# Kernel tuning notes

Measured on AMD Instinct MI355X. Metric: run time of the kernel, lower is better.

Reference implementation:

```python
import jax, jax.numpy as jnp
import numpy as np

B, L, D, H = 2, 2048, 1024, 16
HD = D // H  # head_dim = 64


def setup_inputs() -> dict:
    key = jax.random.key(0)
    ks = jax.random.split(key, 6)
    return {
        "q": jax.random.normal(ks[0], (B, L, D), dtype=jnp.float32),
        "k": jax.random.normal(ks[1], (B, L, D), dtype=jnp.float32),
        "v": jax.random.normal(ks[2], (B, L, D), dtype=jnp.float32),
        "Wq": jax.random.normal(ks[3], (D, D), dtype=jnp.float32) * (D ** -0.5),
        "Wk": jax.random.normal(ks[4], (D, D), dtype=jnp.float32) * (D ** -0.5),
        "Wv": jax.random.normal(ks[5], (D, D), dtype=jnp.float32) * (D ** -0.5),
    }


def reference(q, k, v, Wq, Wk, Wv):
    # nn.Linear(bias=False): y = x @ W.T ; then split heads -> [B,H,L,HD]
    def proj(x, W):
        return (x @ W.T).reshape(B, L, H, HD).transpose(0, 2, 1, 3)

    Q = proj(q, Wq)
    K = proj(k, Wk)
    V = proj(v, Wv)
    scale = HD ** -0.5
    idx = jnp.arange(L)
    # flex_attention score_mod: score + (q_idx - kv_idx), applied after scaling
    bias = (idx[:, None] - idx[None, :]).astype(q.dtype)  # [L, L]
    scores = jnp.einsum('bhqd,bhkd->bhqk', Q, K) * scale + bias
    attn = jax.nn.softmax(scores, axis=-1)
    out = jnp.einsum('bhqk,bhkd->bhqd', attn, V)
    # 'b h l d -> b l (h d)'
    return out.transpose(0, 2, 1, 3).reshape(B, L, D)
```

## Files before the change

### kernel.cpp

```cpp
#include <hip/hip_runtime.h>

#define DEVFN __device__ __forceinline__

typedef __attribute__((ext_vector_type(8))) short bf16x8;
typedef __attribute__((ext_vector_type(4))) float f32x4;

constexpr int cB = 2, cL = 2048, cD = 1024, cH = 16, cHD = 64;
constexpr int ELE   = 4194304;
constexpr int WELE  = 1048576;
constexpr int KWIN  = 128;
constexpr int SLICE = 2 * KWIN * cD;

#if __has_builtin(__builtin_amdgcn_exp2f)
#define EXP2F(x) __builtin_amdgcn_exp2f(x)
#else
#define EXP2F(x) __expf(0.6931471805599453f * (x))
#endif

DEVFN unsigned short hu(float f) {
  return (unsigned short)((__float_as_uint(f) + 0x8000u) >> 16);
}
DEVFN unsigned pkhu(float a, float b) {
  unsigned ua = __float_as_uint(a) + 0x8000u;
  unsigned ub = __float_as_uint(b) + 0x8000u;
  return __builtin_amdgcn_perm(ub, ua, 0x07060302u);
}

#if __has_builtin(__builtin_amdgcn_global_load_lds)
#define HAVE_ASYNC 1
typedef const __attribute__((address_space(1))) unsigned int* gas1_t;
typedef __attribute__((address_space(3))) unsigned int* las3_t;
#define ASYNC_CP16(g, l) \
  __builtin_amdgcn_global_load_lds((gas1_t)(g), (las3_t)(l), 16, 0, 0)
#else
#define HAVE_ASYNC 0
#endif

DEVFN int swzofs(int row, int cc) { return row * 64 + (((cc) ^ (row & 7)) << 3); }

__global__ __launch_bounds__(256)
void conv_bf16(const float* __restrict__ q, const float* __restrict__ k,
               const float* __restrict__ v, const float* __restrict__ Wq,
               const float* __restrict__ Wk, const float* __restrict__ Wv,
               unsigned short* __restrict__ qb, unsigned short* __restrict__ kb,
               unsigned short* __restrict__ vb, unsigned short* __restrict__ wb) {
  const int y = blockIdx.y;
  const int i8 = (blockIdx.x * 256 + threadIdx.x) * 8;
  const float* src; unsigned short* dst; int n;
  size_t sofs = i8, dofs = i8;
  switch (y) {
    case 0:  src = q;  dst = qb;          n = ELE;  break;
    case 1:  case 2: {
      n = SLICE;
      const size_t b = (size_t)(i8 >> 17);
      sofs = b * ((size_t)cL * cD) + (i8 & (KWIN * cD - 1));
      src = (y == 1) ? k : v;  dst = (y == 1) ? kb : vb;  break;
    }
    case 3:  src = Wq; dst = wb;          n = WELE; break;
    case 4:  src = Wk; dst = wb + WELE;   n = WELE; break;
    default: src = Wv; dst = wb + 2*WELE; n = WELE; break;
  }
  if (i8 >= n) return;
  float4 a = *(const float4*)(src + sofs);
  float4 b4 = *(const float4*)(src + sofs + 4);
  uint4 o = {pkhu(a.x, a.y), pkhu(a.z, a.w), pkhu(b4.x, b4.y), pkhu(b4.z, b4.w)};
  *(uint4*)(dst + dofs) = o;
}

__global__ __launch_bounds__(256)
void proj_kv(const unsigned short* __restrict__ xk,
             const unsigned short* __restrict__ xv,
             const unsigned short* __restrict__ wAll,
             unsigned short* __restrict__ Kc,
             unsigned short* __restrict__ Vc) {
  __shared__ __align__(16) unsigned short As[128 * 64];
  __shared__ __align__(16) unsigned short Bs[64 * 64];
  const int tid = threadIdx.x;
  const int wv = tid >> 6, lane = tid & 63, id = lane & 15, quad = lane >> 4;
  const int wr = wv >> 1, wc = wv & 1;
  const int rl = lane >> 3, cc = (lane & 7) ^ rl;

  const int bx = blockIdx.x;
  int mode, M0, N0;
  const unsigned short *A, *B;
  unsigned short* outp;
  if (bx < 32) {
    mode = 1; A = xk; B = wAll + WELE; outp = Kc;
    M0 = (bx & 1) * KWIN;
    N0 = (bx >> 1) * 64;
  } else {
    const int t = bx - 32;
    mode = 2; A = wAll + 2 * WELE; B = xv; outp = Vc;
    M0 = (t & 7) * 128;
    const int y = t >> 3;
    N0 = (y >> 1) * KWIN + (y & 1) * 64;
  }

  f32x4 acc[4][2];
#pragma unroll
  for (int i = 0; i < 4; ++i)
#pragma unroll
    for (int j = 0; j < 2; ++j) acc[i][j] = (f32x4){0.f, 0.f, 0.f, 0.f};

  for (int k0 = 0; k0 < cD; k0 += 64) {
#if HAVE_ASYNC
    __syncthreads();
#pragma unroll
    for (int c = 0; c < 4; ++c)
      ASYNC_CP16(A + (size_t)(M0 + c * 32 + wv * 8 + rl) * cD + k0 + cc * 8,
                 &As[(c * 32 + wv * 8) * 64]);
#pragma unroll
    for (int c = 0; c < 2; ++c)
      ASYNC_CP16(B + (size_t)(N0 + c * 32 + wv * 8 + rl) * cD + k0 + cc * 8,
                 &Bs[(c * 32 + wv * 8) * 64]);
    __syncthreads();
#else
    uint4 ra[4], rb[2];
#pragma unroll
    for (int c = 0; c < 4; ++c)
      ra[c] = *(const uint4*)(A + (size_t)(M0 + c * 32 + wv * 8 + rl) * cD + k0 + cc * 8);
#pragma unroll
    for (int c = 0; c < 2; ++c)
      rb[c] = *(const uint4*)(B + (size_t)(N0 + c * 32 + wv * 8 + rl) * cD + k0 + cc * 8);
    __syncthreads();
#pragma unroll
    for (int c = 0; c < 4; ++c) *(uint4*)&As[(c * 32 + wv * 8) * 64 + lane * 8] = ra[c];
#pragma unroll
    for (int c = 0; c < 2; ++c) *(uint4*)&Bs[(c * 32 + wv * 8) * 64 + lane * 8] = rb[c];
    __syncthreads();
#endif

#pragma unroll
    for (int ks = 0; ks < 2; ++ks) {
      bf16x8 af[4], bfr[2];
#pragma unroll
      for (int mi = 0; mi < 4; ++mi)
        af[mi] = *(const bf16x8*)&As[swzofs(wr * 64 + mi * 16 + id, ks * 4 + quad)];
#pragma unroll
      for (int ni = 0; ni < 2; ++ni)
        bfr[ni] = *(const bf16x8*)&Bs[swzofs(wc * 32 + ni * 16 + id, ks * 4 + quad)];
#pragma unroll
      for (int mi = 0; mi < 4; ++mi)
#pragma unroll
        for (int ni = 0; ni < 2; ++ni)
          acc[mi][ni] = __builtin_amdgcn_mfma_f32_16x16x32_bf16(
              af[mi], bfr[ni], acc[mi][ni], 0, 0, 0);
    }
  }

#pragma unroll
  for (int mi = 0; mi < 4; ++mi) {
#pragma unroll
    for (int ni = 0; ni < 2; ++ni) {
#pragma unroll
      for (int rg = 0; rg < 4; ++rg) {
        const int mr = M0 + wr * 64 + mi * 16 + quad * 4 + rg;
        const int nc = N0 + wc * 32 + ni * 16 + id;
        size_t idx;
        if (mode == 1) {
          const int b = mr >> 7, l = mr & 127, h = nc >> 6, hd = nc & 63;
          idx = ((size_t)((b * cH + h) * KWIN + l)) * cHD + hd;
        } else {
          const int h = mr >> 6, hd = mr & 63, b = nc >> 7, l = nc & 127;
          idx = ((size_t)((b * cH + h) * cHD + hd)) * KWIN + l;
        }
        outp[idx] = hu(acc[mi][ni][rg]);
      }
    }
  }
}

__global__ __launch_bounds__(512)
void fused_qattn(const unsigned short* __restrict__ Xq,
                 const unsigned short* __restrict__ Wq,
                 const unsigned short* __restrict__ Kc,
                 const unsigned short* __restrict__ Vc,
                 float* __restrict__ out) {
  __shared__ __align__(16) unsigned short lds[40960];
  unsigned short* Ks = lds + 24576;
  unsigned short* Vs = lds + 32768;
  unsigned short* Ps = lds + 16384;

  const int tid = threadIdx.x;
  const int wv = tid >> 6, lane = tid & 63, id = lane & 15, quad = lane >> 4;
  const int wr = wv >> 1, wc = wv & 1;
  const int rl = lane >> 3, cc = (lane & 7) ^ rl;
  const int bh = blockIdx.y, q0 = blockIdx.x * 128;
  const int bb = bh >> 4, h = bh & 15;
  const size_t M0 = (size_t)bb * cL + q0;
  const unsigned short* Bw = Wq + (size_t)(h * cHD) * cD;
  const unsigned short* Kb = Kc + (size_t)bh * KWIN * cHD;
  const unsigned short* Vb = Vc + (size_t)bh * cHD * KWIN;

  const int rbase = wv * 8;

#if HAVE_ASYNC
#pragma unroll
  for (int c = 0; c < 2; ++c)
    ASYNC_CP16(Kb + (size_t)(c * 64 + rbase + rl) * cHD + cc * 8,
               &Ks[(c * 64 + rbase) * 64]);
#pragma unroll
  for (int it = 0; it < 2; ++it)
    ASYNC_CP16(Vb + (size_t)(rbase + rl) * KWIN + it * 64 + cc * 8,
               &Vs[it * 4096 + rbase * 64]);
#else
  {
    uint4 kv0r = *(const uint4*)(Kb + (size_t)(rbase + rl) * cHD + cc * 8);
    uint4 kv1r = *(const uint4*)(Kb + (size_t)(64 + rbase + rl) * cHD + cc * 8);
    uint4 vv0r = *(const uint4*)(Vb + (size_t)(rbase + rl) * KWIN + cc * 8);
    uint4 vv1r = *(const uint4*)(Vb + (size_t)(rbase + rl) * KWIN + 64 + cc * 8);
    *(uint4*)&Ks[rbase * 64 + lane * 8] = kv0r;
    *(uint4*)&Ks[(64 + rbase) * 64 + lane * 8] = kv1r;
    *(uint4*)&Vs[rbase * 64 + lane * 8] = vv0r;
    *(uint4*)&Vs[4096 + rbase * 64 + lane * 8] = vv1r;
  }
#endif

#if HAVE_ASYNC
#define STAGE_TILE(buf, k0)                                                    \
  {                                                                            \
    unsigned short* A_ = lds + (buf) * 8192;                                   \
    unsigned short* B_ = lds + 16384 + (buf) * 4096;                           \
    _Pragma("unroll")                                                          \
    for (int c = 0; c < 2; ++c)                                                \
      ASYNC_CP16(Xq + (M0 + c * 64 + wv * 8 + rl) * cD + (k0) + cc * 8,        \
                 &A_[(c * 64 + wv * 8) * 64]);                                 \
    ASYNC_CP16(Bw + (size_t)(wv * 8 + rl) * cD + (k0) + cc * 8,                \
               &B_[(wv * 8) * 64]);                                            \
  }
#else
#define STAGE_TILE(buf, k0)                                                    \
  {                                                                            \
    unsigned short* A_ = lds + (buf) * 8192;                                   \
    unsigned short* B_ = lds + 16384 + (buf) * 4096;                           \
    uint4 ra0 = *(const uint4*)(Xq + (M0 + 0 * 64 + wv * 8 + rl) * cD + (k0) + cc * 8); \
    uint4 ra1 = *(const uint4*)(Xq + (M0 + 1 * 64 + wv * 8 + rl) * cD + (k0) + cc * 8); \
    uint4 rb1 = *(const uint4*)(Bw + (size_t)(wv * 8 + rl) * cD + (k0) + cc * 8);       \
    *(uint4*)&A_[(0 * 64 + wv * 8) * 64 + lane * 8] = ra0;                     \
    *(uint4*)&A_[(1 * 64 + wv * 8) * 64 + lane * 8] = ra1;                     \
    *(uint4*)&B_[(wv * 8) * 64 + lane * 8] = rb1;                              \
  }
#endif

  f32x4 acc[2][2];
#pragma unroll
  for (int i = 0; i < 2; ++i)
#pragma unroll
    for (int j = 0; j < 2; ++j) acc[i][j] = (f32x4){0.f, 0.f, 0.f, 0.f};

  STAGE_TILE(0, 0);
  __syncthreads();

#pragma unroll
  for (int t = 0; t < 16; ++t) {
    const int cur = t & 1;
    if (t < 15) STAGE_TILE(cur ^ 1, (t + 1) * 64);

    const unsigned short* A_ = lds + cur * 8192;
    const unsigned short* B_ = lds + 16384 + cur * 4096;
#pragma unroll
    for (int ks = 0; ks < 2; ++ks) {
      bf16x8 af[2], bfr[2];
#pragma unroll
      for (int mi = 0; mi < 2; ++mi)
        af[mi] = *(const bf16x8*)&A_[swzofs(wr * 32 + mi * 16 + id, ks * 4 + quad)];
#pragma unroll
      for (int ni = 0; ni < 2; ++ni)
        bfr[ni] = *(const bf16x8*)&B_[swzofs(wc * 32 + ni * 16 + id, ks * 4 + quad)];
#pragma unroll
      for (int mi = 0; mi < 2; ++mi)
#pragma unroll
        for (int ni = 0; ni < 2; ++ni)
          acc[mi][ni] = __builtin_amdgcn_mfma_f32_16x16x32_bf16(
              af[mi], bfr[ni], acc[mi][ni], 0, 0, 0);
    }
    __syncthreads();
  }

#pragma unroll
  for (int mi = 0; mi < 2; ++mi)
#pragma unroll
    for (int ni = 0; ni < 2; ++ni)
#pragma unroll
      for (int rg = 0; rg < 4; ++rg) {
        const int qrow = wr * 32 + mi * 16 + quad * 4 + rg;
        const int col  = wc * 32 + ni * 16 + id;
        lds[swzofs(qrow, col >> 3) + (col & 7)] = hu(acc[mi][ni][rg]);
      }
  __syncthreads();

  bf16x8 aq[2];
#pragma unroll
  for (int ks = 0; ks < 2; ++ks)
    aq[ks] = *(const bf16x8*)&lds[swzofs(wv * 16 + id, ks * 4 + quad)];

  constexpr float L2E = 1.4426950408889634f;
  constexpr float SC2 = 0.125f * L2E;

  f32x4 oacc[4];
#pragma unroll
  for (int i = 0; i < 4; ++i) oacc[i] = (f32x4){0.f, 0.f, 0.f, 0.f};
  float m_i[4], l_i[4];
#pragma unroll
  for (int i = 0; i < 4; ++i) { m_i[i] = -1e30f; l_i[i] = 0.f; }

  for (int it = 0; it < 2; ++it) {
    const int kv0 = it * 64;

    f32x4 sa[4];
#pragma unroll
    for (int nt = 0; nt < 4; ++nt) sa[nt] = (f32x4){0.f, 0.f, 0.f, 0.f};
#pragma unroll
    for (int ks = 0; ks < 2; ++ks)
#pragma unroll
      for (int nt = 0; nt < 4; ++nt) {
        bf16x8 kf = *(const bf16x8*)&Ks[swzofs(kv0 + nt * 16 + id, ks * 4 + quad)];
        sa[nt] = __builtin_amdgcn_mfma_f32_16x16x32_bf16(aq[ks], kf, sa[nt], 0, 0, 0);
      }

    const float tkv = (float)(kv0 + id) * L2E;
    float negkb[4];
#pragma unroll
    for (int nt = 0; nt < 4; ++nt) negkb[nt] = -(tkv + (float)(nt * 16) * L2E);

    float z[4][4], mt[4];
#pragma unroll
    for (int i = 0; i < 4; ++i) {
#pragma unroll
      for (int nt = 0; nt < 4; ++nt)
        z[i][nt] = fmaf(sa[nt][i], SC2, negkb[nt]);
      mt[i] = fmaxf(fmaxf(z[i][0], z[i][1]), fmaxf(z[i][2], z[i][3]));
    }
#pragma unroll
    for (int mk = 1; mk < 16; mk <<= 1)
#pragma unroll
      for (int i = 0; i < 4; ++i)
        mt[i] = fmaxf(mt[i], __shfl_xor(mt[i], mk));

    float p[4][4], rs[4], al[4];
#pragma unroll
    for (int i = 0; i < 4; ++i) {
      const float mn = fmaxf(m_i[i], mt[i]);
      al[i] = EXP2F(m_i[i] - mn);
      m_i[i] = mn;
      float s = 0.f;
#pragma unroll
      for (int nt = 0; nt < 4; ++nt) { p[i][nt] = EXP2F(z[i][nt] - mn); s += p[i][nt]; }
      rs[i] = s;
    }
#pragma unroll
    for (int mk = 1; mk < 16; mk <<= 1)
#pragma unroll
      for (int i = 0; i < 4; ++i) rs[i] += __shfl_xor(rs[i], mk);
#pragma unroll
    for (int i = 0; i < 4; ++i) l_i[i] = l_i[i] * al[i] + rs[i];
#pragma unroll
    for (int nh = 0; nh < 4; ++nh)
#pragma unroll
      for (int i = 0; i < 4; ++i) oacc[nh][i] *= al[i];

#pragma unroll
    for (int i = 0; i < 4; ++i) {
      const int qrow = wv * 16 + quad * 4 + i;
#pragma unroll
      for (int nt = 0; nt < 4; ++nt) {
        const int col = nt * 16 + id;
        Ps[swzofs(qrow, col >> 3) + (col & 7)] = hu(p[i][nt]);
      }
    }

    bf16x8 pf[2];
#pragma unroll
    for (int ks2 = 0; ks2 < 2; ++ks2)
      pf[ks2] = *(const bf16x8*)&Ps[swzofs(wv * 16 + id, ks2 * 4 + quad)];
#pragma unroll
    for (int ks2 = 0; ks2 < 2; ++ks2)
#pragma unroll
      for (int nh = 0; nh < 4; ++nh) {
        bf16x8 vf = *(const bf16x8*)&Vs[it * 4096 + swzofs(nh * 16 + id, ks2 * 4 + quad)];
        oacc[nh] = __builtin_amdgcn_mfma_f32_16x16x32_bf16(pf[ks2], vf, oacc[nh], 0, 0, 0);
      }
  }

#pragma unroll
  for (int i = 0; i < 4; ++i) {
    const float inv = 1.0f / l_i[i];
    const int qrow = q0 + wv * 16 + quad * 4 + i;
    float* op = out + ((size_t)(bb * cL + qrow)) * cD + h * cHD + id;
#pragma unroll
    for (int nh = 0; nh < 4; ++nh)
      op[nh * 16] = oacc[nh][i] * inv;
  }
}

extern "C" void kernel_launch(void* const* d_in, const int* in_sizes, int n_in,
                              void* d_out, int out_size, void* d_ws, size_t ws_size,
                              hipStream_t stream) {
  const float* q  = (const float*)d_in[0];
  const float* k  = (const float*)d_in[1];
  const float* v  = (const float*)d_in[2];
  const float* Wq = (const float*)d_in[3];
  const float* Wk = (const float*)d_in[4];
  const float* Wv = (const float*)d_in[5];
  float* out = (float*)d_out;

  unsigned short* Qb  = (unsigned short*)d_ws;
  unsigned short* Wb  = Qb + ELE;
  unsigned short* Ksl = Wb + 3 * WELE;
  unsigned short* Vsl = Ksl + SLICE;
  unsigned short* Kc  = Vsl + SLICE;
  unsigned short* Vc  = Kc + SLICE;

  conv_bf16<<<dim3(2048, 6), dim3(256), 0, stream>>>(q, k, v, Wq, Wk, Wv,
                                                     Qb, Ksl, Vsl, Wb);
  proj_kv<<<dim3(64), dim3(256), 0, stream>>>(Ksl, Vsl, Wb, Kc, Vc);
  fused_qattn<<<dim3(16, 32), dim3(512), 0, stream>>>(Qb, Wb, Kc, Vc, out);
}
```

Measured before the change: 133.1 us.

## Load Q-projection A fragments directly from global into registers, stage only W

The fused Q-projection GEMM now gives each wave its own 16 query rows and reads the A operand (bf16 Q input) straight from global memory into register fragments, double-buffered in registers. Only the weight tile is staged through LDS, with the K step widened to 128. The LDS buffer shrinks and the sync before reading the projected Q is removed, since each wave reads back only its own rows. The cost is more global loads with poor coalescing per wave and higher register pressure.

```diff
diff --git a/kernel.cpp b/kernel.cpp
--- a/kernel.cpp
+++ b/kernel.cpp
@@ -9,7 +9,7 @@
 constexpr int ELE   = 4194304;
 constexpr int WELE  = 1048576;
 constexpr int KWIN  = 128;
-constexpr int SLICE = 2 * KWIN * cD;
+constexpr int SLICE = 262144;
 
 #if __has_builtin(__builtin_amdgcn_exp2f)
 #define EXP2F(x) __builtin_amdgcn_exp2f(x)
@@ -24,6 +24,9 @@
   unsigned ua = __float_as_uint(a) + 0x8000u;
   unsigned ub = __float_as_uint(b) + 0x8000u;
   return __builtin_amdgcn_perm(ub, ua, 0x07060302u);
+}
+DEVFN uint4 pk8(float4 a, float4 b) {
+  return (uint4){pkhu(a.x, a.y), pkhu(a.z, a.w), pkhu(b.x, b.y), pkhu(b.z, b.w)};
 }
 
 #if __has_builtin(__builtin_amdgcn_global_load_lds)
@@ -47,7 +50,7 @@
   const int y = blockIdx.y;
   const int i8 = (blockIdx.x * 256 + threadIdx.x) * 8;
   const float* src; unsigned short* dst; int n;
-  size_t sofs = i8, dofs = i8;
+  size_t sofs = i8;
   switch (y) {
     case 0:  src = q;  dst = qb;          n = ELE;  break;
     case 1:  case 2: {
@@ -63,8 +66,7 @@
   if (i8 >= n) return;
   float4 a = *(const float4*)(src + sofs);
   float4 b4 = *(const float4*)(src + sofs + 4);
-  uint4 o = {pkhu(a.x, a.y), pkhu(a.z, a.w), pkhu(b4.x, b4.y), pkhu(b4.z, b4.w)};
-  *(uint4*)(dst + dofs) = o;
+  *(uint4*)(dst + i8) = pk8(a, b4);
 }
 
 __global__ __launch_bounds__(256)
@@ -171,24 +173,24 @@
 }
 
 __global__ __launch_bounds__(512)
-void fused_qattn(const unsigned short* __restrict__ Xq,
-                 const unsigned short* __restrict__ Wq,
+void fused_qattn(const unsigned short* __restrict__ Qb,
+                 const unsigned short* __restrict__ Wqb,
                  const unsigned short* __restrict__ Kc,
                  const unsigned short* __restrict__ Vc,
                  float* __restrict__ out) {
-  __shared__ __align__(16) unsigned short lds[40960];
-  unsigned short* Ks = lds + 24576;
-  unsigned short* Vs = lds + 32768;
-  unsigned short* Ps = lds + 16384;
+  __shared__ __align__(16) unsigned short lds[32768];
+  unsigned short* Ks = lds + 16384;
+  unsigned short* Vs = lds + 24576;
+  unsigned short* Ps = lds;
 
   const int tid = threadIdx.x;
   const int wv = tid >> 6, lane = tid & 63, id = lane & 15, quad = lane >> 4;
-  const int wr = wv >> 1, wc = wv & 1;
   const int rl = lane >> 3, cc = (lane & 7) ^ rl;
   const int bh = blockIdx.y, q0 = blockIdx.x * 128;
   const int bb = bh >> 4, h = bh & 15;
-  const size_t M0 = (size_t)bb * cL + q0;
-  const unsigned short* Bw = Wq + (size_t)(h * cHD) * cD;
+  const unsigned short* Arow =
+      Qb + (size_t)(bb * cL + q0 + wv * 16 + id) * cD;
+  const unsigned short* Bw = Wqb + (size_t)(h * cHD) * cD;
   const unsigned short* Kb = Kc + (size_t)bh * KWIN * cHD;
   const unsigned short* Vb = Vc + (size_t)bh * cHD * KWIN;
 
@@ -217,82 +219,68 @@
 #endif
 
 #if HAVE_ASYNC
-#define STAGE_TILE(buf, k0)                                                    \
+#define STAGE_B(buf, k0)                                                       \
   {                                                                            \
-    unsigned short* A_ = lds + (buf) * 8192;                                   \
-    unsigned short* B_ = lds + 16384 + (buf) * 4096;                           \
     _Pragma("unroll")                                                          \
-    for (int c = 0; c < 2; ++c)                                                \
-      ASYNC_CP16(Xq + (M0 + c * 64 + wv * 8 + rl) * cD + (k0) + cc * 8,        \
-                 &A_[(c * 64 + wv * 8) * 64]);                                 \
-    ASYNC_CP16(Bw + (size_t)(wv * 8 + rl) * cD + (k0) + cc * 8,                \
-               &B_[(wv * 8) * 64]);                                            \
+    for (int h_ = 0; h_ < 2; ++h_)                                             \
+      ASYNC_CP16(Bw + (size_t)(wv * 8 + rl) * cD + (k0) + h_ * 64 + cc * 8,    \
+                 &lds[(buf) * 8192 + h_ * 4096 + (wv * 8) * 64]);              \
   }
 #else
-#define STAGE_TILE(buf, k0)                                                    \
+#define STAGE_B(buf, k0)                                                       \
   {                                                                            \
-    unsigned short* A_ = lds + (buf) * 8192;                                   \
-    unsigned short* B_ = lds + 16384 + (buf) * 4096;                           \
-    uint4 ra0 = *(const uint4*)(Xq + (M0 + 0 * 64 + wv * 8 + rl) * cD + (k0) + cc * 8); \
-    uint4 ra1 = *(const uint4*)(Xq + (M0 + 1 * 64 + wv * 8 + rl) * cD + (k0) + cc * 8); \
-    uint4 rb1 = *(const uint4*)(Bw + (size_t)(wv * 8 + rl) * cD + (k0) + cc * 8);       \
-    *(uint4*)&A_[(0 * 64 + wv * 8) * 64 + lane * 8] = ra0;                     \
-    *(uint4*)&A_[(1 * 64 + wv * 8) * 64 + lane * 8] = ra1;                     \
-    *(uint4*)&B_[(wv * 8) * 64 + lane * 8] = rb1;                              \
+    _Pragma("unroll")                                                          \
+    for (int h_ = 0; h_ < 2; ++h_) {                                           \
+      uint4 rb_ = *(const uint4*)(Bw + (size_t)(wv * 8 + rl) * cD + (k0) + h_ * 64 + cc * 8); \
+      *(uint4*)&lds[(buf) * 8192 + h_ * 4096 + (wv * 8) * 64 + lane * 8] = rb_; \
+    }                                                                          \
   }
 #endif
 
-  f32x4 acc[2][2];
-#pragma unroll
-  for (int i = 0; i < 2; ++i)
-#pragma unroll
-    for (int j = 0; j < 2; ++j) acc[i][j] = (f32x4){0.f, 0.f, 0.f, 0.f};
-
-  STAGE_TILE(0, 0);
+  f32x4 acc[4];
+#pragma unroll
+  for (int i = 0; i < 4; ++i) acc[i] = (f32x4){0.f, 0.f, 0.f, 0.f};
+
+  bf16x8 afr[2][4];
+#pragma unroll
+  for (int ks = 0; ks < 4; ++ks)
+    afr[0][ks] = *(const bf16x8*)(Arow + ks * 32 + quad * 8);
+  STAGE_B(0, 0);
   __syncthreads();
 
 #pragma unroll
-  for (int t = 0; t < 16; ++t) {
+  for (int t = 0; t < 8; ++t) {
     const int cur = t & 1;
-    if (t < 15) STAGE_TILE(cur ^ 1, (t + 1) * 64);
-
-    const unsigned short* A_ = lds + cur * 8192;
-    const unsigned short* B_ = lds + 16384 + cur * 4096;
-#pragma unroll
-    for (int ks = 0; ks < 2; ++ks) {
-      bf16x8 af[2], bfr[2];
-#pragma unroll
-      for (int mi = 0; mi < 2; ++mi)
-        af[mi] = *(const bf16x8*)&A_[swzofs(wr * 32 + mi * 16 + id, ks * 4 + quad)];
-#pragma unroll
-      for (int ni = 0; ni < 2; ++ni)
-        bfr[ni] = *(const bf16x8*)&B_[swzofs(wc * 32 + ni * 16 + id, ks * 4 + quad)];
-#pragma unroll
-      for (int mi = 0; mi < 2; ++mi)
-#pragma unroll
-        for (int ni = 0; ni < 2; ++ni)
-          acc[mi][ni] = __builtin_amdgcn_mfma_f32_16x16x32_bf16(
-              af[mi], bfr[ni], acc[mi][ni], 0, 0, 0);
+    if (t < 7) {
+      STAGE_B(cur ^ 1, (t + 1) * 128);
+#pragma unroll
+      for (int ks = 0; ks < 4; ++ks)
+        afr[cur ^ 1][ks] = *(const bf16x8*)(Arow + (t + 1) * 128 + ks * 32 + quad * 8);
+    }
+#pragma unroll
+    for (int ks = 0; ks < 4; ++ks) {
+#pragma unroll
+      for (int nt = 0; nt < 4; ++nt) {
+        bf16x8 bfr = *(const bf16x8*)&lds[cur * 8192 + (ks >> 1) * 4096 +
+                                          swzofs(nt * 16 + id, (ks & 1) * 4 + quad)];
+        acc[nt] = __builtin_amdgcn_mfma_f32_16x16x32_bf16(afr[cur][ks], bfr, acc[nt], 0, 0, 0);
+      }
     }
     __syncthreads();
   }
 
 #pragma unroll
-  for (int mi = 0; mi < 2; ++mi)
-#pragma unroll
-    for (int ni = 0; ni < 2; ++ni)
-#pragma unroll
-      for (int rg = 0; rg < 4; ++rg) {
-        const int qrow = wr * 32 + mi * 16 + quad * 4 + rg;
-        const int col  = wc * 32 + ni * 16 + id;
-        lds[swzofs(qrow, col >> 3) + (col & 7)] = hu(acc[mi][ni][rg]);
-      }
-  __syncthreads();
-
+  for (int nt = 0; nt < 4; ++nt)
+#pragma unroll
+    for (int rg = 0; rg < 4; ++rg) {
+      const int qrow = wv * 16 + quad * 4 + rg;
+      const int col  = nt * 16 + id;
+      Ps[swzofs(qrow, col >> 3) + (col & 7)] = hu(acc[nt][rg]);
+    }
   bf16x8 aq[2];
 #pragma unroll
   for (int ks = 0; ks < 2; ++ks)
-    aq[ks] = *(const bf16x8*)&lds[swzofs(wv * 16 + id, ks * 4 + quad)];
+    aq[ks] = *(const bf16x8*)&Ps[swzofs(wv * 16 + id, ks * 4 + quad)];
 
   constexpr float L2E = 1.4426950408889634f;
   constexpr float SC2 = 0.125f * L2E;
```

New measurement: 139.4 us. +4.8%, slower.
